# Kernel tuning notes

Hardware: AMD Instinct MI355X
Metric: run time of the kernel (lower is better)

## Reference

```python
import jax, jax.numpy as jnp
import numpy as np

D_MODEL = 1024
N_HEADS = 16
D_K = D_MODEL // N_HEADS
D_FF = 4096
B, S = 4, 2048


def setup_inputs() -> dict:
    key = jax.random.key(0)
    ks = jax.random.split(key, 16)
    s = 0.02
    inp = {
        "x": jax.random.normal(ks[0], (B, S, D_MODEL), dtype=jnp.float32),
        "wq": jax.random.normal(ks[1], (D_MODEL, D_MODEL), dtype=jnp.float32) * s,
        "bq": jnp.zeros((D_MODEL,), jnp.float32),
        "wk": jax.random.normal(ks[2], (D_MODEL, D_MODEL), dtype=jnp.float32) * s,
        "bk": jnp.zeros((D_MODEL,), jnp.float32),
        "wv": jax.random.normal(ks[3], (D_MODEL, D_MODEL), dtype=jnp.float32) * s,
        "bv": jnp.zeros((D_MODEL,), jnp.float32),
        "wo": jax.random.normal(ks[4], (D_MODEL, D_MODEL), dtype=jnp.float32) * s,
        "bo": jnp.zeros((D_MODEL,), jnp.float32),
        "w1": jax.random.normal(ks[5], (D_MODEL, D_FF), dtype=jnp.float32) * s,
        "b1": jnp.zeros((D_FF,), jnp.float32),
        "w2": jax.random.normal(ks[6], (D_FF, D_MODEL), dtype=jnp.float32) * s,
        "b2": jnp.zeros((D_MODEL,), jnp.float32),
        "ln1_g": jnp.ones((D_MODEL,), jnp.float32),
        "ln1_b": jnp.zeros((D_MODEL,), jnp.float32),
        "ln2_g": jnp.ones((D_MODEL,), jnp.float32),
        "ln2_b": jnp.zeros((D_MODEL,), jnp.float32),
    }
    return inp


def _layernorm(x, g, b, eps=1e-5):
    mu = jnp.mean(x, axis=-1, keepdims=True)
    var = jnp.mean(jnp.square(x - mu), axis=-1, keepdims=True)
    return (x - mu) * jax.lax.rsqrt(var + eps) * g + b


def _attention(h, wq, bq, wk, bk, wv, bv, wo, bo):
    b, s, _ = h.shape
    q = (h @ wq + bq).reshape(b, s, N_HEADS, D_K).transpose(0, 2, 1, 3)
    k = (h @ wk + bk).reshape(b, s, N_HEADS, D_K).transpose(0, 2, 1, 3)
    v = (h @ wv + bv).reshape(b, s, N_HEADS, D_K).transpose(0, 2, 1, 3)
    scores = jnp.einsum('bhqd,bhkd->bhqk', q, k) / jnp.sqrt(jnp.float32(D_K))
    causal = jnp.triu(jnp.ones((s, s), dtype=bool), k=1)  # True above diag
    scores = jnp.where(causal[None, None], -jnp.inf, scores)
    attn = jax.nn.softmax(scores, axis=-1)
    out = jnp.einsum('bhqk,bhkd->bhqd', attn, v)
    out = out.transpose(0, 2, 1, 3).reshape(b, s, D_MODEL)
    return out @ wo + bo


def reference(x, wq, bq, wk, bk, wv, bv, wo, bo, w1, b1, w2, b2,
              ln1_g, ln1_b, ln2_g, ln2_b):
    attn_out = _attention(_layernorm(x, ln1_g, ln1_b), wq, bq, wk, bk, wv, bv, wo, bo)
    x = x + attn_out
    h = _layernorm(x, ln2_g, ln2_b)
    ff = jax.nn.gelu(h @ w1 + b1, approximate=False) @ w2 + b2
    return x + ff
```

## Files before the change

### kernel.cpp

```cpp
#include <hip/hip_runtime.h>
#include <hip/hip_bf16.h>

#define DM   1024
#define DFF  4096
#define NB   4
#define SS   2048
#define NH   16
#define DK   64
#define MROWS (NB*SS)

typedef __attribute__((ext_vector_type(8))) short bfx8;
typedef __attribute__((ext_vector_type(4))) float fx4;
typedef unsigned int u32;
typedef unsigned short u16;

static __device__ __forceinline__ u16 f2bf(float f) {
  union { __hip_bfloat16 h; u16 u; } cv;
  cv.h = __float2bfloat16(f);
  return cv.u;
}
static __device__ __forceinline__ u32 pk2bf(float a, float b) {
  return (u32)f2bf(a) | ((u32)f2bf(b) << 16);
}

static __device__ __forceinline__ void async16(void* lds, const void* g) {
  typedef const __attribute__((address_space(1))) unsigned int* gp_t;
  typedef __attribute__((address_space(3))) unsigned int* lp_t;
  __builtin_amdgcn_global_load_lds((gp_t)g, (lp_t)lds, 16, 0, 0);
}

__global__ __launch_bounds__(256) void k_transpose(const float* __restrict__ in,
                                                   u16* __restrict__ out,
                                                   int K, int N) {
  __shared__ float t[32][33];
  const int n0 = blockIdx.x * 32, k0 = blockIdx.y * 32;
  const int tx = threadIdx.x & 31, ty = threadIdx.x >> 5;
#pragma unroll
  for (int j = 0; j < 4; j++)
    t[ty + j * 8][tx] = in[(size_t)(k0 + ty + j * 8) * N + n0 + tx];
  __syncthreads();
#pragma unroll
  for (int j = 0; j < 4; j++)
    out[(size_t)(n0 + ty + j * 8) * K + k0 + tx] = f2bf(t[tx][ty + j * 8]);
}

__global__ __launch_bounds__(256) void k_layernorm(const float* __restrict__ x,
                                                   const float* __restrict__ g,
                                                   const float* __restrict__ b,
                                                   u16* __restrict__ out) {
  const int row  = blockIdx.x * 4 + (threadIdx.x >> 6);
  const int lane = threadIdx.x & 63;
  const float* xr = x + (size_t)row * DM;
  float4 vb[4];
  float s = 0.f, s2 = 0.f;
#pragma unroll
  for (int j = 0; j < 4; j++) {
    float4 v = *(const float4*)(xr + j * 256 + lane * 4);
    vb[j] = v;
    s  += v.x + v.y + v.z + v.w;
    s2 += v.x * v.x + v.y * v.y + v.z * v.z + v.w * v.w;
  }
#pragma unroll
  for (int off = 1; off < 64; off <<= 1) {
    s  += __shfl_xor(s,  off);
    s2 += __shfl_xor(s2, off);
  }
  const float mu   = s * (1.f / DM);
  const float var  = s2 * (1.f / DM) - mu * mu;
  const float rstd = rsqrtf(var + 1e-5f);
  u16* orow = out + (size_t)row * DM;
#pragma unroll
  for (int j = 0; j < 4; j++) {
    const int col = j * 256 + lane * 4;
    uint2 o;
    o.x = pk2bf((vb[j].x - mu) * rstd * g[col + 0] + b[col + 0],
                (vb[j].y - mu) * rstd * g[col + 1] + b[col + 1]);
    o.y = pk2bf((vb[j].z - mu) * rstd * g[col + 2] + b[col + 2],
                (vb[j].w - mu) * rstd * g[col + 3] + b[col + 3]);
    *(uint2*)(orow + col) = o;
  }
}

template <int EPI>
__global__ __launch_bounds__(256) void k_gemm_bt(const u16* __restrict__ A,
                                                 const u16* __restrict__ BT,
                                                 const float* __restrict__ bias0,
                                                 const float* __restrict__ bias1,
                                                 const float* __restrict__ bias2,
                                                 const float* __restrict__ res,
                                                 void* __restrict__ outp,
                                                 int M, int N, int K) {
  __shared__ u16 Al[128 * 64];
  __shared__ u16 Bl[128 * 64];
  const int tid = threadIdx.x, wave = tid >> 6, lane = tid & 63;
  const int nwg = gridDim.x * gridDim.y;
  const int bid = blockIdx.y * gridDim.x + blockIdx.x;
  const int swz = (bid & 7) * (nwg >> 3) + (bid >> 3);
  const int m0 = (swz / gridDim.x) * 128, n0 = (swz % gridDim.x) * 128;
  const int wm = (wave >> 1) * 64, wn = (wave & 1) * 64;
  const int la = lane & 15, lg = lane >> 4;
  fx4 acc[4][4];
#pragma unroll
  for (int i = 0; i < 4; i++)
#pragma unroll
    for (int j = 0; j < 4; j++) acc[i][j] = fx4{0.f, 0.f, 0.f, 0.f};

  const int srow = lane >> 3;
  const int sslot = (lane & 7) ^ srow;
  const u16* ga = A  + (size_t)(m0 + wave * 32 + srow) * K + sslot * 8;
  const u16* gb = BT + (size_t)(n0 + wave * 32 + srow) * K + sslot * 8;
  char* lA = (char*)Al + wave * 4096;
  char* lB = (char*)Bl + wave * 4096;
  const int sw = la & 7;

  for (int k0 = 0; k0 < K; k0 += 64) {
#pragma unroll
    for (int i = 0; i < 4; i++) async16(lA + i * 1024, ga + (size_t)(i * 8) * K + k0);
#pragma unroll
    for (int i = 0; i < 4; i++) async16(lB + i * 1024, gb + (size_t)(i * 8) * K + k0);
    __syncthreads();
#pragma unroll
    for (int kk = 0; kk < 2; kk++) {
      bfx8 av[4], bv[4];
#pragma unroll
      for (int mt = 0; mt < 4; mt++)
        av[mt] = *(const bfx8*)((const char*)Al + (wm + mt * 16 + la) * 128 +
                                (((kk << 2) + lg) ^ sw) * 16);
#pragma unroll
      for (int nt = 0; nt < 4; nt++)
        bv[nt] = *(const bfx8*)((const char*)Bl + (wn + nt * 16 + la) * 128 +
                                (((kk << 2) + lg) ^ sw) * 16);
      __builtin_amdgcn_s_setprio(1);
#pragma unroll
      for (int mt = 0; mt < 4; mt++)
#pragma unroll
        for (int nt = 0; nt < 4; nt++)
          acc[mt][nt] = __builtin_amdgcn_mfma_f32_16x16x32_bf16(av[mt], bv[nt], acc[mt][nt], 0, 0, 0);
      __builtin_amdgcn_s_setprio(0);
    }
    __syncthreads();
  }

  if constexpr (EPI == 4) {
    const int reg = n0 >> 10;
    const float* bp = (reg == 0) ? bias0 : (reg == 1) ? bias1 : bias2;
#pragma unroll
    for (int nt = 0; nt < 4; nt++) {
      const int n  = n0 + wn + nt * 16 + la;
      const int nl = n & 1023;
      const float bs = bp[nl];
      if (reg < 2) {
        u16* base = (u16*)outp + (size_t)reg * (8u * 1024 * 1024);
#pragma unroll
        for (int mt = 0; mt < 4; mt++)
#pragma unroll
          for (int vv = 0; vv < 4; vv++) {
            const int m = m0 + wm + mt * 16 + lg * 4 + vv;
            base[(size_t)m * 1024 + nl] = f2bf(acc[mt][nt][vv] + bs);
          }
      } else {
        const int hh = nl >> 6, d = nl & 63;
#pragma unroll
        for (int mt = 0; mt < 4; mt++) {
          const int m = m0 + wm + mt * 16 + lg * 4;
          const int bb = m >> 11, s = m & 2047;
          u16* vp = (u16*)outp + 16u * 1024 * 1024 +
                    (((size_t)bb * NH + hh) * DK + d) * SS + s;
          uint2 o;
          o.x = pk2bf(acc[mt][nt][0] + bs, acc[mt][nt][1] + bs);
          o.y = pk2bf(acc[mt][nt][2] + bs, acc[mt][nt][3] + bs);
          *(uint2*)vp = o;
        }
      }
    }
  } else {
#pragma unroll
    for (int nt = 0; nt < 4; nt++) {
      const int n = n0 + wn + nt * 16 + la;
      const float bs = bias0[n];
#pragma unroll
      for (int mt = 0; mt < 4; mt++) {
#pragma unroll
        for (int vv = 0; vv < 4; vv++) {
          const int m = m0 + wm + mt * 16 + lg * 4 + vv;
          const float val = acc[mt][nt][vv] + bs;
          const size_t idx = (size_t)m * N + n;
          if constexpr (EPI == 1) {
            ((float*)outp)[idx] = res[idx] + val;
          } else {
            const float gl = 0.5f * val * (1.f + erff(val * 0.70710678118f));
            ((u16*)outp)[idx] = f2bf(gl);
          }
        }
      }
    }
  }
}

__global__ __launch_bounds__(512, 4) void k_attn(const u16* __restrict__ q,
                                                 const u16* __restrict__ k,
                                                 const u16* __restrict__ vt,
                                                 u16* __restrict__ att) {
  __shared__ char sm[65536];
  const int bid = blockIdx.x;
  const int bq = 15 - (bid >> 6);
  const int bh = bid & 63;
  const int b = bh >> 4, h = bh & 15;

  const int tid = threadIdx.x, wave = tid >> 6, lane = tid & 63;
  const int g = wave >> 2, wv4 = wave & 3;
  const int la = lane & 15, lg = lane >> 4;
  const int q0 = bq * 128;

  bfx8 qf[2][2];
#pragma unroll
  for (int qt = 0; qt < 2; qt++) {
    const u16* qp = q + (size_t)(b * SS + q0 + wv4 * 32 + qt * 16 + la) * DM + h * DK + lg * 8;
#pragma unroll
    for (int f = 0; f < 2; f++) qf[qt][f] = *(const bfx8*)(qp + f * 32);
  }

  fx4 acc[2][4];
#pragma unroll
  for (int qt = 0; qt < 2; qt++)
#pragma unroll
    for (int dt = 0; dt < 4; dt++) acc[qt][dt] = fx4{0.f, 0.f, 0.f, 0.f};
  float mold[2] = {-10000.f, -10000.f};
  float lsum[2] = {0.f, 0.f};

  const int srow = lane >> 3;
  const int sslot = (lane & 7) ^ srow;
  const u16* kg0 = k  + (size_t)(b * SS + wv4 * 16 + srow) * DM + h * DK + sslot * 8;
  const u16* vg0 = vt + (size_t)((b * NH + h) * DK + wv4 * 16 + srow) * SS + sslot * 8;
  char* kbase = sm + g * 32768 + wv4 * 2048;
  char* vbase = sm + g * 32768 + 16384 + wv4 * 2048;

  const float c1 = 0.18033688f;
  const int niter = bq + 1;

  auto stage = [&](int buf, int i) {
    const int c0 = (2 * i + g) * 64;
#pragma unroll
    for (int j = 0; j < 2; j++)
      async16(kbase + buf * 8192 + j * 1024, kg0 + (size_t)(c0 + j * 8) * DM);
#pragma unroll
    for (int j = 0; j < 2; j++)
      async16(vbase + buf * 8192 + j * 1024, vg0 + (size_t)(j * 8) * SS + c0);
  };

  stage(0, 0);
  int cur = 0;
  const int sw = la & 7;

  for (int i = 0; i < niter; i++) {
    __syncthreads();
    if (i + 1 < niter) stage(cur ^ 1, i + 1);
    const int c0 = (2 * i + g) * 64;
    const bool msk = (i == niter - 1);
    const char* Kb = sm + g * 32768 + cur * 8192;
    const char* Vb = sm + g * 32768 + 16384 + cur * 8192;

    fx4 st[2][4];
    __builtin_amdgcn_s_setprio(1);
#pragma unroll
    for (int t = 0; t < 4; t++) {
      const char* kr = Kb + (size_t)(t * 16 + la) * 128;
      bfx8 kf0 = *(const bfx8*)(kr + ((0 + lg) ^ sw) * 16);
      bfx8 kf1 = *(const bfx8*)(kr + ((4 + lg) ^ sw) * 16);
#pragma unroll
      for (int qt = 0; qt < 2; qt++) {
        fx4 z = fx4{0.f, 0.f, 0.f, 0.f};
        z = __builtin_amdgcn_mfma_f32_16x16x32_bf16(kf0, qf[qt][0], z, 0, 0, 0);
        z = __builtin_amdgcn_mfma_f32_16x16x32_bf16(kf1, qf[qt][1], z, 0, 0, 0);
        st[qt][t] = z;
      }
    }
    __builtin_amdgcn_s_setprio(0);

    if (msk) {
#pragma unroll
      for (int qt = 0; qt < 2; qt++) {
        const int qir = q0 + wv4 * 32 + qt * 16 + la;
#pragma unroll
        for (int t = 0; t < 4; t++)
#pragma unroll
          for (int r = 0; r < 4; r++)
            if (c0 + t * 16 + lg * 4 + r > qir) st[qt][t][r] = -1e9f;
      }
    }

    float lmx[2];
#pragma unroll
    for (int qt = 0; qt < 2; qt++) {
      float mx = fmaxf(fmaxf(st[qt][0][0], st[qt][0][1]), fmaxf(st[qt][0][2], st[qt][0][3]));
#pragma unroll
      for (int t = 1; t < 4; t++)
        mx = fmaxf(mx, fmaxf(fmaxf(st[qt][t][0], st[qt][t][1]), fmaxf(st[qt][t][2], st[qt][t][3])));
      lmx[qt] = mx * c1;
    }
    const bool def = (lmx[0] <= mold[0] + 8.f) && (lmx[1] <= mold[1] + 8.f);
    if (!__all(def)) {
#pragma unroll
      for (int qt = 0; qt < 2; qt++) {
        float mx = lmx[qt];
        mx = fmaxf(mx, __shfl_xor(mx, 16));
        mx = fmaxf(mx, __shfl_xor(mx, 32));
        const float mnew  = fmaxf(mold[qt], mx);
        const float scale = exp2f(mold[qt] - mnew);
        mold[qt] = mnew;
        lsum[qt] *= scale;
#pragma unroll
        for (int dt = 0; dt < 4; dt++) {
          acc[qt][dt][0] *= scale; acc[qt][dt][1] *= scale;
          acc[qt][dt][2] *= scale; acc[qt][dt][3] *= scale;
        }
      }
    }
    u32 W[2][4][2];
#pragma unroll
    for (int qt = 0; qt < 2; qt++) {
      float ps = 0.f;
#pragma unroll
      for (int t = 0; t < 4; t++) {
        float p0 = exp2f(fmaf(st[qt][t][0], c1, -mold[qt]));
        float p1 = exp2f(fmaf(st[qt][t][1], c1, -mold[qt]));
        float p2 = exp2f(fmaf(st[qt][t][2], c1, -mold[qt]));
        float p3 = exp2f(fmaf(st[qt][t][3], c1, -mold[qt]));
        ps += (p0 + p1) + (p2 + p3);
        W[qt][t][0] = pk2bf(p0, p1);
        W[qt][t][1] = pk2bf(p2, p3);
      }
      lsum[qt] += ps;
    }

    const int sLo = la + ((lg & 1) << 5);
    const int sHi = sLo + 16;
    const bool tHi = (lg >> 1) & 1;
#pragma unroll
    for (int f = 0; f < 2; f++) {
      bfx8 pf[2];
#pragma unroll
      for (int qt = 0; qt < 2; qt++) {
        const u32 a0 = __shfl(W[qt][2 * f][0], sLo), b0 = __shfl(W[qt][2 * f + 1][0], sLo);
        const u32 a1 = __shfl(W[qt][2 * f][1], sLo), b1 = __shfl(W[qt][2 * f + 1][1], sLo);
        const u32 a2 = __shfl(W[qt][2 * f][0], sHi), b2 = __shfl(W[qt][2 * f + 1][0], sHi);
        const u32 a3 = __shfl(W[qt][2 * f][1], sHi), b3 = __shfl(W[qt][2 * f + 1][1], sHi);
        union { u32 u[4]; bfx8 v; } pu;
        pu.u[0] = tHi ? b0 : a0;
        pu.u[1] = tHi ? b1 : a1;
        pu.u[2] = tHi ? b2 : a2;
        pu.u[3] = tHi ? b3 : a3;
        pf[qt] = pu.v;
      }
      __builtin_amdgcn_s_setprio(1);
#pragma unroll
      for (int dt = 0; dt < 4; dt++) {
        const int row = dt * 16 + la;
        bfx8 vf = *(const bfx8*)(Vb + (size_t)row * 128 + (((f << 2) + lg) ^ sw) * 16);
        acc[0][dt] = __builtin_amdgcn_mfma_f32_16x16x32_bf16(vf, pf[0], acc[0][dt], 0, 0, 0);
        acc[1][dt] = __builtin_amdgcn_mfma_f32_16x16x32_bf16(vf, pf[1], acc[1][dt], 0, 0, 0);
      }
      __builtin_amdgcn_s_setprio(0);
    }
    cur ^= 1;
  }

#pragma unroll
  for (int qt = 0; qt < 2; qt++) {
    lsum[qt] += __shfl_xor(lsum[qt], 16);
    lsum[qt] += __shfl_xor(lsum[qt], 32);
  }

  __syncthreads();
  const int gi = wv4 * 64 + lane;
  float* scr = (float*)sm + (size_t)gi * 36;
  if (g == 1) {
#pragma unroll
    for (int qt = 0; qt < 2; qt++)
#pragma unroll
      for (int dt = 0; dt < 4; dt++)
#pragma unroll
        for (int j = 0; j < 4; j++) scr[qt * 16 + dt * 4 + j] = acc[qt][dt][j];
    scr[32] = mold[0]; scr[33] = mold[1];
    scr[34] = lsum[0]; scr[35] = lsum[1];
  }
  __syncthreads();
  if (g == 0) {
#pragma unroll
    for (int qt = 0; qt < 2; qt++) {
      const float mB = scr[32 + qt], lB = scr[34 + qt];
      const float mN = fmaxf(mold[qt], mB);
      const float sA = exp2f(mold[qt] - mN);
      const float sB = exp2f(mB - mN);
      const float inv = 1.f / (lsum[qt] * sA + lB * sB);
      u16* ob = att + (size_t)(b * SS + q0 + wv4 * 32 + qt * 16 + la) * DM + h * DK + lg * 4;
#pragma unroll
      for (int dt = 0; dt < 4; dt++) {
        float o0 = (acc[qt][dt][0] * sA + scr[qt * 16 + dt * 4 + 0] * sB) * inv;
        float o1 = (acc[qt][dt][1] * sA + scr[qt * 16 + dt * 4 + 1] * sB) * inv;
        float o2 = (acc[qt][dt][2] * sA + scr[qt * 16 + dt * 4 + 2] * sB) * inv;
        float o3 = (acc[qt][dt][3] * sA + scr[qt * 16 + dt * 4 + 3] * sB) * inv;
        uint2 o;
        o.x = pk2bf(o0, o1);
        o.y = pk2bf(o2, o3);
        *(uint2*)(ob + dt * 16) = o;
      }
    }
  }
}

extern "C" void kernel_launch(void* const* d_in, const int* in_sizes, int n_in,
                              void* d_out, int out_size, void* d_ws, size_t ws_size,
                              hipStream_t stream) {
  const float* x    = (const float*)d_in[0];
  const float* wq   = (const float*)d_in[1];
  const float* bq   = (const float*)d_in[2];
  const float* wk   = (const float*)d_in[3];
  const float* bk   = (const float*)d_in[4];
  const float* wv   = (const float*)d_in[5];
  const float* bv   = (const float*)d_in[6];
  const float* wo   = (const float*)d_in[7];
  const float* bo   = (const float*)d_in[8];
  const float* w1   = (const float*)d_in[9];
  const float* b1   = (const float*)d_in[10];
  const float* w2   = (const float*)d_in[11];
  const float* b2   = (const float*)d_in[12];
  const float* ln1g = (const float*)d_in[13];
  const float* ln1b = (const float*)d_in[14];
  const float* ln2g = (const float*)d_in[15];
  const float* ln2b = (const float*)d_in[16];
  float* out = (float*)d_out;

  char* w = (char*)d_ws;
  const size_t MB = 1024ull * 1024ull;
  u16*   wqkv = (u16*)(w + 0 * MB);
  u16*   wot  = (u16*)(w + 6 * MB);
  u16*   w1t  = (u16*)(w + 8 * MB);
  u16*   w2t  = (u16*)(w + 16 * MB);
  float* x2   = (float*)(w + 24 * MB);
  u16*   hb   = (u16*)(w + 56 * MB);
  u16*   qb   = (u16*)(w + 72 * MB);
  u16*   kb   = (u16*)(w + 88 * MB);
  u16*   vtb  = (u16*)(w + 104 * MB);
  u16*   atb  = (u16*)(w + 120 * MB);
  u16*   ffb  = (u16*)(w + 72 * MB);

  k_transpose<<<dim3(32, 32),  256, 0, stream>>>(wq, wqkv,               1024, 1024);
  k_transpose<<<dim3(32, 32),  256, 0, stream>>>(wk, wqkv + 1024 * 1024, 1024, 1024);
  k_transpose<<<dim3(32, 32),  256, 0, stream>>>(wv, wqkv + 2048 * 1024, 1024, 1024);
  k_transpose<<<dim3(32, 32),  256, 0, stream>>>(wo, wot, 1024, 1024);
  k_transpose<<<dim3(128, 32), 256, 0, stream>>>(w1, w1t, 1024, 4096);
  k_transpose<<<dim3(32, 128), 256, 0, stream>>>(w2, w2t, 4096, 1024);

  k_layernorm<<<MROWS / 4, 256, 0, stream>>>(x, ln1g, ln1b, hb);

  k_gemm_bt<4><<<dim3(24, 64), 256, 0, stream>>>(hb, wqkv, bq, bk, bv, nullptr, qb,
                                                 MROWS, 3 * DM, DM);

  k_attn<<<dim3(1024), 512, 0, stream>>>(qb, kb, vtb, atb);

  k_gemm_bt<1><<<dim3(8, 64), 256, 0, stream>>>(atb, wot, bo, nullptr, nullptr, x, x2,
                                                MROWS, DM, DM);

  k_layernorm<<<MROWS / 4, 256, 0, stream>>>(x2, ln2g, ln2b, hb);

  k_gemm_bt<2><<<dim3(32, 64), 256, 0, stream>>>(hb, w1t, b1, nullptr, nullptr, nullptr, ffb,
                                                 MROWS, DFF, DM);

  k_gemm_bt<1><<<dim3(8, 64), 256, 0, stream>>>(ffb, w2t, b2, nullptr, nullptr, x2, out,
                                                MROWS, DM, DFF);
}
```

Measured before the change: 405.7 us.

## Double-buffer GEMM LDS tiles with async prefetch two stages ahead

Doubles the LDS A/B tile buffers in the bf16 GEMM and issues async global-to-LDS loads for the tile two steps ahead, waiting on vmcnt only for the current tile. The goal is to overlap global memory latency with the MFMA work instead of stalling on every K step. It doubles LDS use per block (64KB), which may lower occupancy, and relies on a hand-written vmcnt count being correct.

```diff
diff --git a/kernel.cpp b/kernel.cpp
--- a/kernel.cpp
+++ b/kernel.cpp
@@ -90,8 +90,8 @@
                                                  const float* __restrict__ res,
                                                  void* __restrict__ outp,
                                                  int M, int N, int K) {
-  __shared__ u16 Al[128 * 64];
-  __shared__ u16 Bl[128 * 64];
+  __shared__ u16 Al[2 * 128 * 64];
+  __shared__ u16 Bl[2 * 128 * 64];
   const int tid = threadIdx.x, wave = tid >> 6, lane = tid & 63;
   const int nwg = gridDim.x * gridDim.y;
   const int bid = blockIdx.y * gridDim.x + blockIdx.x;
@@ -113,22 +113,37 @@
   char* lB = (char*)Bl + wave * 4096;
   const int sw = la & 7;
 
-  for (int k0 = 0; k0 < K; k0 += 64) {
-#pragma unroll
-    for (int i = 0; i < 4; i++) async16(lA + i * 1024, ga + (size_t)(i * 8) * K + k0);
-#pragma unroll
-    for (int i = 0; i < 4; i++) async16(lB + i * 1024, gb + (size_t)(i * 8) * K + k0);
-    __syncthreads();
+  auto stageg = [&](int buf, int k0) {
+#pragma unroll
+    for (int i = 0; i < 4; i++)
+      async16(lA + buf * 16384 + i * 1024, ga + (size_t)(i * 8) * K + k0);
+#pragma unroll
+    for (int i = 0; i < 4; i++)
+      async16(lB + buf * 16384 + i * 1024, gb + (size_t)(i * 8) * K + k0);
+  };
+
+  const int nk = K >> 6;
+  stageg(0, 0);
+  stageg(1, 64);
+  int cur = 0;
+
+  for (int t = 0; t < nk; ++t) {
+    if (t < nk - 1) { asm volatile("s_waitcnt vmcnt(8)" ::: "memory"); }
+    else            { asm volatile("s_waitcnt vmcnt(0)" ::: "memory"); }
+    __builtin_amdgcn_s_barrier();
+    asm volatile("" ::: "memory");
+    const char* Ab = (const char*)Al + cur * 16384;
+    const char* Bb = (const char*)Bl + cur * 16384;
 #pragma unroll
     for (int kk = 0; kk < 2; kk++) {
       bfx8 av[4], bv[4];
 #pragma unroll
       for (int mt = 0; mt < 4; mt++)
-        av[mt] = *(const bfx8*)((const char*)Al + (wm + mt * 16 + la) * 128 +
+        av[mt] = *(const bfx8*)(Ab + (wm + mt * 16 + la) * 128 +
                                 (((kk << 2) + lg) ^ sw) * 16);
 #pragma unroll
       for (int nt = 0; nt < 4; nt++)
-        bv[nt] = *(const bfx8*)((const char*)Bl + (wn + nt * 16 + la) * 128 +
+        bv[nt] = *(const bfx8*)(Bb + (wn + nt * 16 + la) * 128 +
                                 (((kk << 2) + lg) ^ sw) * 16);
       __builtin_amdgcn_s_setprio(1);
 #pragma unroll
@@ -138,7 +153,10 @@
           acc[mt][nt] = __builtin_amdgcn_mfma_f32_16x16x32_bf16(av[mt], bv[nt], acc[mt][nt], 0, 0, 0);
       __builtin_amdgcn_s_setprio(0);
     }
-    __syncthreads();
+    asm volatile("" ::: "memory");
+    __builtin_amdgcn_s_barrier();
+    if (t + 2 < nk) stageg(cur, (t + 2) << 6);
+    cur ^= 1;
   }
 
   if constexpr (EPI == 4) {
```

New measurement: 398.1 us. Within noise of the previous version (-1.9%).

## Rework GEMM into larger 512-thread tiles with a 4-stage async LDS pipeline

Applied to the files above, without the earlier changes.

The bf16 GEMM kernel moves from 128x128 tiles with 256 threads and a single-buffered K=64 loop to 256xBN tiles with 512 threads (configurable wave grid). It adds a 4-deep ring of K=32 LDS stages and uses explicit vmcnt waits, so global loads for future stages overlap the MFMA work and there is one barrier per step. Larger tiles raise data reuse per workgroup. The trade-offs are fewer workgroups on the smaller GEMMs, more LDS and registers per block, and dropping the XOR LDS swizzle, which may cause bank conflicts.

```diff
diff --git a/kernel.cpp b/kernel.cpp
--- a/kernel.cpp
+++ b/kernel.cpp
@@ -81,64 +81,88 @@
   }
 }
 
-template <int EPI>
-__global__ __launch_bounds__(256) void k_gemm_bt(const u16* __restrict__ A,
-                                                 const u16* __restrict__ BT,
-                                                 const float* __restrict__ bias0,
-                                                 const float* __restrict__ bias1,
-                                                 const float* __restrict__ bias2,
-                                                 const float* __restrict__ res,
-                                                 void* __restrict__ outp,
-                                                 int M, int N, int K) {
-  __shared__ u16 Al[128 * 64];
-  __shared__ u16 Bl[128 * 64];
+template <int EPI, int NWR>
+__global__ __launch_bounds__(512, 2) void k_gemm_bt(const u16* __restrict__ A,
+                                                    const u16* __restrict__ BT,
+                                                    const float* __restrict__ bias0,
+                                                    const float* __restrict__ bias1,
+                                                    const float* __restrict__ bias2,
+                                                    const float* __restrict__ res,
+                                                    void* __restrict__ outp,
+                                                    int M, int N, int K) {
+  constexpr int NWC    = 8 / NWR;
+  constexpr int BN     = NWC * 64;
+  constexpr int MFRAG  = 256 / NWR / 16;
+  constexpr int ABYTES = 256 * 32 * 2;
+  constexpr int BBYTES = BN * 32 * 2;
+  constexpr int LA     = ABYTES / (512 * 16);
+  constexpr int LB     = BBYTES / (512 * 16);
+  constexpr int L      = LA + LB;
+
+  __shared__ char Al[4 * ABYTES];
+  __shared__ char Bl[4 * BBYTES];
+
   const int tid = threadIdx.x, wave = tid >> 6, lane = tid & 63;
   const int nwg = gridDim.x * gridDim.y;
   const int bid = blockIdx.y * gridDim.x + blockIdx.x;
   const int swz = (bid & 7) * (nwg >> 3) + (bid >> 3);
-  const int m0 = (swz / gridDim.x) * 128, n0 = (swz % gridDim.x) * 128;
-  const int wm = (wave >> 1) * 64, wn = (wave & 1) * 64;
+  const int m0 = (swz / gridDim.x) * 256, n0 = (swz % gridDim.x) * BN;
+  const int wr = wave / NWC, wc = wave % NWC;
+  const int wm = wr * (256 / NWR), wn = wc * 64;
   const int la = lane & 15, lg = lane >> 4;
-  fx4 acc[4][4];
-#pragma unroll
-  for (int i = 0; i < 4; i++)
+
+  fx4 acc[MFRAG][4];
+#pragma unroll
+  for (int i = 0; i < MFRAG; i++)
 #pragma unroll
     for (int j = 0; j < 4; j++) acc[i][j] = fx4{0.f, 0.f, 0.f, 0.f};
 
-  const int srow = lane >> 3;
-  const int sslot = (lane & 7) ^ srow;
-  const u16* ga = A  + (size_t)(m0 + wave * 32 + srow) * K + sslot * 8;
-  const u16* gb = BT + (size_t)(n0 + wave * 32 + srow) * K + sslot * 8;
-  char* lA = (char*)Al + wave * 4096;
-  char* lB = (char*)Bl + wave * 4096;
-  const int sw = la & 7;
-
-  for (int k0 = 0; k0 < K; k0 += 64) {
-#pragma unroll
-    for (int i = 0; i < 4; i++) async16(lA + i * 1024, ga + (size_t)(i * 8) * K + k0);
-#pragma unroll
-    for (int i = 0; i < 4; i++) async16(lB + i * 1024, gb + (size_t)(i * 8) * K + k0);
-    __syncthreads();
-#pragma unroll
-    for (int kk = 0; kk < 2; kk++) {
-      bfx8 av[4], bv[4];
-#pragma unroll
-      for (int mt = 0; mt < 4; mt++)
-        av[mt] = *(const bfx8*)((const char*)Al + (wm + mt * 16 + la) * 128 +
-                                (((kk << 2) + lg) ^ sw) * 16);
+  const int arow = tid >> 2, aslot = (tid & 3) * 8;
+  const u16* gA = A  + (size_t)(m0 + arow) * K + aslot;
+  const u16* gB = BT + (size_t)(n0 + arow) * K + aslot;
+
+  auto stageg = [&](int buf, int kt) {
+#pragma unroll
+    for (int j = 0; j < LA; j++)
+      async16(Al + buf * ABYTES + j * 8192 + wave * 1024, gA + (size_t)(j * 128) * K + kt);
+#pragma unroll
+    for (int j = 0; j < LB; j++)
+      async16(Bl + buf * BBYTES + j * 8192 + wave * 1024, gB + (size_t)(j * 128) * K + kt);
+  };
+
+  const int nk = K >> 5;
+  stageg(0, 0);
+  stageg(1, 32);
+  stageg(2, 64);
+
+  for (int t = 0; t < nk; ++t) {
+    const int rem = nk - 1 - t;
+    if (rem >= 2)      { asm volatile("s_waitcnt vmcnt(%0)" :: "n"(2 * L) : "memory"); }
+    else if (rem == 1) { asm volatile("s_waitcnt vmcnt(%0)" :: "n"(L)     : "memory"); }
+    else               { asm volatile("s_waitcnt vmcnt(0)" ::: "memory"); }
+    __builtin_amdgcn_s_barrier();
+    asm volatile("" ::: "memory");
+
+    const char* Ab = (const char*)Al + (t & 3) * ABYTES;
+    const char* Bb = (const char*)Bl + (t & 3) * BBYTES;
+    bfx8 av[MFRAG], bv[4];
+#pragma unroll
+    for (int mt = 0; mt < MFRAG; mt++)
+      av[mt] = *(const bfx8*)(Ab + (wm + mt * 16 + la) * 64 + lg * 16);
+#pragma unroll
+    for (int nt = 0; nt < 4; nt++)
+      bv[nt] = *(const bfx8*)(Bb + (wn + nt * 16 + la) * 64 + lg * 16);
+
+    if (t + 3 < nk) stageg((t + 3) & 3, (t + 3) * 32);
+
+    __builtin_amdgcn_s_setprio(1);
+#pragma unroll
+    for (int mt = 0; mt < MFRAG; mt++)
 #pragma unroll
       for (int nt = 0; nt < 4; nt++)
-        bv[nt] = *(const bfx8*)((const char*)Bl + (wn + nt * 16 + la) * 128 +
-                                (((kk << 2) + lg) ^ sw) * 16);
-      __builtin_amdgcn_s_setprio(1);
-#pragma unroll
-      for (int mt = 0; mt < 4; mt++)
-#pragma unroll
-        for (int nt = 0; nt < 4; nt++)
-          acc[mt][nt] = __builtin_amdgcn_mfma_f32_16x16x32_bf16(av[mt], bv[nt], acc[mt][nt], 0, 0, 0);
-      __builtin_amdgcn_s_setprio(0);
-    }
-    __syncthreads();
+        acc[mt][nt] = __builtin_amdgcn_mfma_f32_16x16x32_bf16(av[mt], bv[nt], acc[mt][nt], 0, 0, 0);
+    __builtin_amdgcn_s_setprio(0);
+    asm volatile("" ::: "memory");
   }
 
   if constexpr (EPI == 4) {
@@ -152,7 +176,7 @@
       if (reg < 2) {
         u16* base = (u16*)outp + (size_t)reg * (8u * 1024 * 1024);
 #pragma unroll
-        for (int mt = 0; mt < 4; mt++)
+        for (int mt = 0; mt < MFRAG; mt++)
 #pragma unroll
           for (int vv = 0; vv < 4; vv++) {
             const int m = m0 + wm + mt * 16 + lg * 4 + vv;
@@ -161,7 +185,7 @@
       } else {
         const int hh = nl >> 6, d = nl & 63;
 #pragma unroll
-        for (int mt = 0; mt < 4; mt++) {
+        for (int mt = 0; mt < MFRAG; mt++) {
           const int m = m0 + wm + mt * 16 + lg * 4;
           const int bb = m >> 11, s = m & 2047;
           u16* vp = (u16*)outp + 16u * 1024 * 1024 +
@@ -179,7 +203,7 @@
       const int n = n0 + wn + nt * 16 + la;
       const float bs = bias0[n];
 #pragma unroll
-      for (int mt = 0; mt < 4; mt++) {
+      for (int mt = 0; mt < MFRAG; mt++) {
 #pragma unroll
         for (int vv = 0; vv < 4; vv++) {
           const int m = m0 + wm + mt * 16 + lg * 4 + vv;
@@ -454,19 +478,19 @@
 
   k_layernorm<<<MROWS / 4, 256, 0, stream>>>(x, ln1g, ln1b, hb);
 
-  k_gemm_bt<4><<<dim3(24, 64), 256, 0, stream>>>(hb, wqkv, bq, bk, bv, nullptr, qb,
-                                                 MROWS, 3 * DM, DM);
+  k_gemm_bt<4, 4><<<dim3(24, 32), 512, 0, stream>>>(hb, wqkv, bq, bk, bv, nullptr, qb,
+                                                    MROWS, 3 * DM, DM);
 
   k_attn<<<dim3(1024), 512, 0, stream>>>(qb, kb, vtb, atb);
 
-  k_gemm_bt<1><<<dim3(8, 64), 256, 0, stream>>>(atb, wot, bo, nullptr, nullptr, x, x2,
-                                                MROWS, DM, DM);
+  k_gemm_bt<1, 4><<<dim3(8, 32), 512, 0, stream>>>(atb, wot, bo, nullptr, nullptr, x, x2,
+                                                   MROWS, DM, DM);
 
   k_layernorm<<<MROWS / 4, 256, 0, stream>>>(x2, ln2g, ln2b, hb);
 
-  k_gemm_bt<2><<<dim3(32, 64), 256, 0, stream>>>(hb, w1t, b1, nullptr, nullptr, nullptr, ffb,
-                                                 MROWS, DFF, DM);
-
-  k_gemm_bt<1><<<dim3(8, 64), 256, 0, stream>>>(ffb, w2t, b2, nullptr, nullptr, x2, out,
-                                                MROWS, DM, DFF);
-}
+  k_gemm_bt<2, 2><<<dim3(16, 32), 512, 0, stream>>>(hb, w1t, b1, nullptr, nullptr, nullptr, ffb,
+                                                    MROWS, DFF, DM);
+
+  k_gemm_bt<1, 4><<<dim3(8, 32), 512, 0, stream>>>(ffb, w2t, b2, nullptr, nullptr, x2, out,
+                                                   MROWS, DM, DFF);
+}
```

Result: no change. 405.3 us (-0.1%).

## Rewrite GEMM as 256x128 pipelined kernel with register-direct B loads

Applied to the files above, without the earlier changes.

The GEMM moves to 512 threads with 256x128 tiles and a four-buffer LDS ring for A, issued through async global-to-LDS loads three tiles ahead. B fragments are loaded straight into registers with inline global_load_dwordx4 and double-buffered, and explicit vmcnt waits replace the full syncthreads pairs. The bf16 epilogues now stage through LDS so that stores are coalesced, and the six weight transposes are merged into one launch. The aim is to hide memory latency and cut barrier and launch overhead, at the cost of fragile hand-counted waitcnt logic and uncoalesced per-lane B loads from global memory.

```diff
diff --git a/kernel.cpp b/kernel.cpp
--- a/kernel.cpp
+++ b/kernel.cpp
@@ -13,6 +13,7 @@
 typedef __attribute__((ext_vector_type(4))) float fx4;
 typedef unsigned int u32;
 typedef unsigned short u16;
+typedef unsigned long long u64;
 
 static __device__ __forceinline__ u16 f2bf(float f) {
   union { __hip_bfloat16 h; u16 u; } cv;
@@ -29,11 +30,28 @@
   __builtin_amdgcn_global_load_lds((gp_t)g, (lp_t)lds, 16, 0, 0);
 }
 
-__global__ __launch_bounds__(256) void k_transpose(const float* __restrict__ in,
-                                                   u16* __restrict__ out,
-                                                   int K, int N) {
+__global__ __launch_bounds__(256) void k_transpose_all(
+    const float* __restrict__ wq, const float* __restrict__ wk,
+    const float* __restrict__ wv, const float* __restrict__ wo,
+    const float* __restrict__ w1, const float* __restrict__ w2,
+    u16* __restrict__ wqkv, u16* __restrict__ wot,
+    u16* __restrict__ w1t,  u16* __restrict__ w2t) {
   __shared__ float t[32][33];
-  const int n0 = blockIdx.x * 32, k0 = blockIdx.y * 32;
+  const int idx = blockIdx.x;
+  const float* in; u16* out; int K, N, bx, by;
+  if (idx < 4096) {
+    const int m = idx >> 10, tl = idx & 1023;
+    in  = (m == 0) ? wq : (m == 1) ? wk : (m == 2) ? wv : wo;
+    out = (m < 3) ? (wqkv + (size_t)m * 1024 * 1024) : wot;
+    K = 1024; N = 1024; bx = tl & 31; by = tl >> 5;
+  } else if (idx < 8192) {
+    const int tl = idx - 4096;
+    in = w1; out = w1t; K = 1024; N = 4096; bx = tl & 127; by = tl >> 7;
+  } else {
+    const int tl = idx - 8192;
+    in = w2; out = w2t; K = 4096; N = 1024; bx = tl & 31; by = tl >> 5;
+  }
+  const int n0 = bx * 32, k0 = by * 32;
   const int tx = threadIdx.x & 31, ty = threadIdx.x >> 5;
 #pragma unroll
   for (int j = 0; j < 4; j++)
@@ -82,7 +100,7 @@
 }
 
 template <int EPI>
-__global__ __launch_bounds__(256) void k_gemm_bt(const u16* __restrict__ A,
+__global__ __launch_bounds__(512) void k_gemm_bt(const u16* __restrict__ A,
                                                  const u16* __restrict__ BT,
                                                  const float* __restrict__ bias0,
                                                  const float* __restrict__ bias1,
@@ -90,82 +108,139 @@
                                                  const float* __restrict__ res,
                                                  void* __restrict__ outp,
                                                  int M, int N, int K) {
-  __shared__ u16 Al[128 * 64];
-  __shared__ u16 Bl[128 * 64];
+  constexpr int ABUF = 256 * 32 * 2;
+  __shared__ char Al[4 * ABUF];
+
   const int tid = threadIdx.x, wave = tid >> 6, lane = tid & 63;
   const int nwg = gridDim.x * gridDim.y;
   const int bid = blockIdx.y * gridDim.x + blockIdx.x;
   const int swz = (bid & 7) * (nwg >> 3) + (bid >> 3);
-  const int m0 = (swz / gridDim.x) * 128, n0 = (swz % gridDim.x) * 128;
-  const int wm = (wave >> 1) * 64, wn = (wave & 1) * 64;
+  const int m0 = (swz / gridDim.x) * 256, n0 = (swz % gridDim.x) * 128;
+  const int wr = wave >> 1, wc = wave & 1;
+  const int wm = wr * 64, wn = wc * 64;
   const int la = lane & 15, lg = lane >> 4;
+  const int psw = (la >> 1) & 3;
+
   fx4 acc[4][4];
 #pragma unroll
   for (int i = 0; i < 4; i++)
 #pragma unroll
     for (int j = 0; j < 4; j++) acc[i][j] = fx4{0.f, 0.f, 0.f, 0.f};
 
-  const int srow = lane >> 3;
-  const int sslot = (lane & 7) ^ srow;
-  const u16* ga = A  + (size_t)(m0 + wave * 32 + srow) * K + sslot * 8;
-  const u16* gb = BT + (size_t)(n0 + wave * 32 + srow) * K + sslot * 8;
-  char* lA = (char*)Al + wave * 4096;
-  char* lB = (char*)Bl + wave * 4096;
-  const int sw = la & 7;
-
-  for (int k0 = 0; k0 < K; k0 += 64) {
-#pragma unroll
-    for (int i = 0; i < 4; i++) async16(lA + i * 1024, ga + (size_t)(i * 8) * K + k0);
-#pragma unroll
-    for (int i = 0; i < 4; i++) async16(lB + i * 1024, gb + (size_t)(i * 8) * K + k0);
-    __syncthreads();
-#pragma unroll
-    for (int kk = 0; kk < 2; kk++) {
-      bfx8 av[4], bv[4];
-#pragma unroll
-      for (int mt = 0; mt < 4; mt++)
-        av[mt] = *(const bfx8*)((const char*)Al + (wm + mt * 16 + la) * 128 +
-                                (((kk << 2) + lg) ^ sw) * 16);
+  const int arow = tid >> 2;
+  const int aslot = ((tid & 3) ^ ((tid >> 3) & 3)) * 8;
+  const u16* gA = A + (size_t)(m0 + arow) * K + aslot;
+
+  auto stageA = [&](int buf, int kt) {
+#pragma unroll
+    for (int j = 0; j < 2; j++)
+      async16(Al + buf * ABUF + j * 8192 + wave * 1024, gA + (size_t)(j * 128) * K + kt);
+  };
+
+  u64 bb[4];
+#pragma unroll
+  for (int nt = 0; nt < 4; nt++)
+    bb[nt] = (u64)(BT + (size_t)(n0 + wn + nt * 16 + la) * K + lg * 8);
+
+  auto loadB = [&](bfx8 (&dst)[4], int kt) {
+#pragma unroll
+    for (int nt = 0; nt < 4; nt++) {
+      u64 a = bb[nt] + (u64)kt * 2;
+      asm volatile("global_load_dwordx4 %0, %1, off"
+                   : "=v"(dst[nt]) : "v"(a) : "memory");
+    }
+  };
+
+  const int nk = K >> 5;
+  bfx8 bA[4], bB[4];
+  loadB(bA, 0);
+  stageA(0, 0);
+  stageA(1, 32);
+  stageA(2, 64);
+  asm volatile("s_waitcnt vmcnt(4)" ::: "memory");
+  __builtin_amdgcn_sched_barrier(0);
+  __builtin_amdgcn_s_barrier();
+  asm volatile("" ::: "memory");
+
+  auto tile = [&](int t, bfx8 (&bcur)[4], bfx8 (&bnext)[4]) {
+    const char* Ab = (const char*)Al + (t & 3) * ABUF;
+    bfx8 av[4];
+#pragma unroll
+    for (int i = 0; i < 4; i++)
+      av[i] = *(const bfx8*)(Ab + (wm + i * 16 + la) * 64 + (lg ^ psw) * 16);
+    if (t + 1 < nk) loadB(bnext, (t + 1) * 32);
+    if (t + 3 < nk) stageA((t + 3) & 3, (t + 3) * 32);
+    __builtin_amdgcn_s_setprio(1);
+#pragma unroll
+    for (int mt = 0; mt < 4; mt++)
 #pragma unroll
       for (int nt = 0; nt < 4; nt++)
-        bv[nt] = *(const bfx8*)((const char*)Bl + (wn + nt * 16 + la) * 128 +
-                                (((kk << 2) + lg) ^ sw) * 16);
-      __builtin_amdgcn_s_setprio(1);
-#pragma unroll
-      for (int mt = 0; mt < 4; mt++)
-#pragma unroll
-        for (int nt = 0; nt < 4; nt++)
-          acc[mt][nt] = __builtin_amdgcn_mfma_f32_16x16x32_bf16(av[mt], bv[nt], acc[mt][nt], 0, 0, 0);
-      __builtin_amdgcn_s_setprio(0);
-    }
-    __syncthreads();
-  }
+        acc[mt][nt] = __builtin_amdgcn_mfma_f32_16x16x32_bf16(av[mt], bcur[nt], acc[mt][nt], 0, 0, 0);
+    __builtin_amdgcn_s_setprio(0);
+    const int rem = nk - 1 - t;
+    if (rem >= 3)      { asm volatile("s_waitcnt vmcnt(2)" ::: "memory"); }
+    else if (rem >= 1) { asm volatile("s_waitcnt vmcnt(0)" ::: "memory"); }
+    __builtin_amdgcn_sched_barrier(0);
+    __builtin_amdgcn_s_barrier();
+    asm volatile("" ::: "memory");
+  };
+
+  for (int t = 0; t < nk; t += 2) {
+    tile(t,     bA, bB);
+    tile(t + 1, bB, bA);
+  }
+
+  float* scr = (float*)(Al) + (size_t)wave * (68 * 16);
+
+  auto emit_bf16 = [&](u16* base, size_t ld, int mrow0, int ncol0,
+                       const float v[4][4] ) {
+#pragma unroll
+    for (int nt = 0; nt < 4; nt++)
+#pragma unroll
+      for (int vv = 0; vv < 4; vv++)
+        scr[(lg * 4 + vv) * 68 + nt * 16 + la] = v[nt][vv];
+    asm volatile("s_waitcnt lgkmcnt(0)" ::: "memory");
+#pragma unroll
+    for (int p = 0; p < 4; p++) {
+      const int r  = p * 4 + (lane >> 4);
+      const int cg = lane & 15;
+      float4 q = *(const float4*)&scr[r * 68 + cg * 4];
+      uint2 o;
+      o.x = pk2bf(q.x, q.y);
+      o.y = pk2bf(q.z, q.w);
+      *(uint2*)(base + (size_t)(mrow0 + r) * ld + ncol0 + cg * 4) = o;
+    }
+    asm volatile("s_waitcnt lgkmcnt(0)" ::: "memory");
+  };
 
   if constexpr (EPI == 4) {
     const int reg = n0 >> 10;
     const float* bp = (reg == 0) ? bias0 : (reg == 1) ? bias1 : bias2;
-#pragma unroll
-    for (int nt = 0; nt < 4; nt++) {
-      const int n  = n0 + wn + nt * 16 + la;
-      const int nl = n & 1023;
-      const float bs = bp[nl];
-      if (reg < 2) {
-        u16* base = (u16*)outp + (size_t)reg * (8u * 1024 * 1024);
-#pragma unroll
-        for (int mt = 0; mt < 4; mt++)
-#pragma unroll
-          for (int vv = 0; vv < 4; vv++) {
-            const int m = m0 + wm + mt * 16 + lg * 4 + vv;
-            base[(size_t)m * 1024 + nl] = f2bf(acc[mt][nt][vv] + bs);
-          }
-      } else {
+    if (reg < 2) {
+      u16* base = (u16*)outp + (size_t)reg * (8u * 1024 * 1024);
+#pragma unroll
+      for (int mt = 0; mt < 4; mt++) {
+        float v[4][4];
+#pragma unroll
+        for (int nt = 0; nt < 4; nt++) {
+          const float bs = bp[(n0 + wn + nt * 16 + la) & 1023];
+#pragma unroll
+          for (int vv = 0; vv < 4; vv++) v[nt][vv] = acc[mt][nt][vv] + bs;
+        }
+        emit_bf16(base, 1024, m0 + wm + mt * 16, (n0 + wn) & 1023, v);
+      }
+    } else {
+#pragma unroll
+      for (int nt = 0; nt < 4; nt++) {
+        const int nl = (n0 + wn + nt * 16 + la) & 1023;
+        const float bs = bp[nl];
         const int hh = nl >> 6, d = nl & 63;
 #pragma unroll
         for (int mt = 0; mt < 4; mt++) {
           const int m = m0 + wm + mt * 16 + lg * 4;
-          const int bb = m >> 11, s = m & 2047;
+          const int bb2 = m >> 11, s = m & 2047;
           u16* vp = (u16*)outp + 16u * 1024 * 1024 +
-                    (((size_t)bb * NH + hh) * DK + d) * SS + s;
+                    (((size_t)bb2 * NH + hh) * DK + d) * SS + s;
           uint2 o;
           o.x = pk2bf(acc[mt][nt][0] + bs, acc[mt][nt][1] + bs);
           o.y = pk2bf(acc[mt][nt][2] + bs, acc[mt][nt][3] + bs);
@@ -173,6 +248,21 @@
         }
       }
     }
+  } else if constexpr (EPI == 2) {
+#pragma unroll
+    for (int mt = 0; mt < 4; mt++) {
+      float v[4][4];
+#pragma unroll
+      for (int nt = 0; nt < 4; nt++) {
+        const float bs = bias0[n0 + wn + nt * 16 + la];
+#pragma unroll
+        for (int vv = 0; vv < 4; vv++) {
+          const float val = acc[mt][nt][vv] + bs;
+          v[nt][vv] = 0.5f * val * (1.f + erff(val * 0.70710678118f));
+        }
+      }
+      emit_bf16((u16*)outp, N, m0 + wm + mt * 16, n0 + wn, v);
+    }
   } else {
 #pragma unroll
     for (int nt = 0; nt < 4; nt++) {
@@ -183,14 +273,8 @@
 #pragma unroll
         for (int vv = 0; vv < 4; vv++) {
           const int m = m0 + wm + mt * 16 + lg * 4 + vv;
-          const float val = acc[mt][nt][vv] + bs;
           const size_t idx = (size_t)m * N + n;
-          if constexpr (EPI == 1) {
-            ((float*)outp)[idx] = res[idx] + val;
-          } else {
-            const float gl = 0.5f * val * (1.f + erff(val * 0.70710678118f));
-            ((u16*)outp)[idx] = f2bf(gl);
-          }
+          ((float*)outp)[idx] = res[idx] + acc[mt][nt][vv] + bs;
         }
       }
     }
@@ -445,28 +529,24 @@
   u16*   atb  = (u16*)(w + 120 * MB);
   u16*   ffb  = (u16*)(w + 72 * MB);
 
-  k_transpose<<<dim3(32, 32),  256, 0, stream>>>(wq, wqkv,               1024, 1024);
-  k_transpose<<<dim3(32, 32),  256, 0, stream>>>(wk, wqkv + 1024 * 1024, 1024, 1024);
-  k_transpose<<<dim3(32, 32),  256, 0, stream>>>(wv, wqkv + 2048 * 1024, 1024, 1024);
-  k_transpose<<<dim3(32, 32),  256, 0, stream>>>(wo, wot, 1024, 1024);
-  k_transpose<<<dim3(128, 32), 256, 0, stream>>>(w1, w1t, 1024, 4096);
-  k_transpose<<<dim3(32, 128), 256, 0, stream>>>(w2, w2t, 4096, 1024);
+  k_transpose_all<<<dim3(12288), 256, 0, stream>>>(wq, wk, wv, wo, w1, w2,
+                                                   wqkv, wot, w1t, w2t);
 
   k_layernorm<<<MROWS / 4, 256, 0, stream>>>(x, ln1g, ln1b, hb);
 
-  k_gemm_bt<4><<<dim3(24, 64), 256, 0, stream>>>(hb, wqkv, bq, bk, bv, nullptr, qb,
+  k_gemm_bt<4><<<dim3(24, 32), 512, 0, stream>>>(hb, wqkv, bq, bk, bv, nullptr, qb,
                                                  MROWS, 3 * DM, DM);
 
   k_attn<<<dim3(1024), 512, 0, stream>>>(qb, kb, vtb, atb);
 
-  k_gemm_bt<1><<<dim3(8, 64), 256, 0, stream>>>(atb, wot, bo, nullptr, nullptr, x, x2,
+  k_gemm_bt<1><<<dim3(8, 32), 512, 0, stream>>>(atb, wot, bo, nullptr, nullptr, x, x2,
                                                 MROWS, DM, DM);
 
   k_layernorm<<<MROWS / 4, 256, 0, stream>>>(x2, ln2g, ln2b, hb);
 
-  k_gemm_bt<2><<<dim3(32, 64), 256, 0, stream>>>(hb, w1t, b1, nullptr, nullptr, nullptr, ffb,
+  k_gemm_bt<2><<<dim3(32, 32), 512, 0, stream>>>(hb, w1t, b1, nullptr, nullptr, nullptr, ffb,
                                                  MROWS, DFF, DM);
 
-  k_gemm_bt<1><<<dim3(8, 64), 256, 0, stream>>>(ffb, w2t, b2, nullptr, nullptr, x2, out,
+  k_gemm_bt<1><<<dim3(8, 32), 512, 0, stream>>>(ffb, w2t, b2, nullptr, nullptr, x2, out,
                                                 MROWS, DM, DFF);
 }
```

After: 629.8 us. 1.55x slower.
